# Performance work log

Hardware: AMD Instinct MI355X
Metric: run time of the kernel (lower is better)

The kernel has to match this reference:

```python
import jax, jax.numpy as jnp
import numpy as np

N = 100000
E = 1600000
IN_DIM = 64
EMB_DIM = 64
BN_EPS = 1e-5


def setup_inputs() -> dict:
    key = jax.random.key(0)
    ks = jax.random.split(key, 8)
    x = jax.random.normal(ks[0], (N, IN_DIM), dtype=jnp.float32)
    edge_index = jax.random.randint(ks[1], (2, E), 0, N, dtype=jnp.int64)
    # GIN learned epsilon (train_eps=True), initialized to 0 as in PyG
    eps = jnp.zeros((), dtype=jnp.float32)
    # MLP params: Linear(in, emb) -> BN -> ReLU -> Linear(emb, emb)
    s1 = 1.0 / np.sqrt(IN_DIM)
    W1 = jax.random.uniform(ks[2], (IN_DIM, EMB_DIM), jnp.float32, -s1, s1)
    b1 = jax.random.uniform(ks[3], (EMB_DIM,), jnp.float32, -s1, s1)
    gamma = jnp.ones((EMB_DIM,), jnp.float32)
    beta = jnp.zeros((EMB_DIM,), jnp.float32)
    s2 = 1.0 / np.sqrt(EMB_DIM)
    W2 = jax.random.uniform(ks[4], (EMB_DIM, EMB_DIM), jnp.float32, -s2, s2)
    b2 = jax.random.uniform(ks[5], (EMB_DIM,), jnp.float32, -s2, s2)
    return {"x": x, "edge_index": edge_index, "eps": eps,
            "W1": W1, "b1": b1, "gamma": gamma, "beta": beta,
            "W2": W2, "b2": b2}


def reference(x, edge_index, eps, W1, b1, gamma, beta, W2, b2):
    src, dst = edge_index[0], edge_index[1]
    # GIN aggregation: sum of neighbor (source) features at each destination
    agg = jax.ops.segment_sum(x[src], dst, num_segments=N)  # [N, IN_DIM]
    h = (1.0 + eps) * x + agg
    # MLP: Linear -> BatchNorm1d (training-mode batch stats) -> ReLU -> Linear
    h1 = h @ W1 + b1                                   # [N, EMB_DIM]
    mean = jnp.mean(h1, axis=0)
    var = jnp.mean((h1 - mean) ** 2, axis=0)           # biased var, as torch BN
    h1n = (h1 - mean) * jax.lax.rsqrt(var + BN_EPS) * gamma + beta
    h2 = jax.nn.relu(h1n)
    return h2 @ W2 + b2                                # [N, EMB_DIM]
```

## Files before the change

### kernel.cpp

```cpp
#include <hip/hip_runtime.h>

#define NNODES 100000
#define NEDGES 1600000
#define DIM 64
#define NB 782
#define NPB 256
#define CHUNK 6250
#define CAP 3968
#define HP 68
#define NTILES 6250

typedef __attribute__((ext_vector_type(4))) float f32x4;
typedef __attribute__((ext_vector_type(8))) short s16x8;

__device__ __forceinline__ unsigned short bf16_rne(float f) {
  unsigned u = __float_as_uint(f);
  u += 0x7FFF + ((u >> 16) & 1);
  return (unsigned short)(u >> 16);
}
__device__ __forceinline__ float bf16_to_f32(unsigned short h) {
  return __uint_as_float(((unsigned)h) << 16);
}

__global__ __launch_bounds__(256) void prep_kernel(
    const float* __restrict__ x, unsigned short* __restrict__ xb,
    int* __restrict__ gcursor, float* __restrict__ sums,
    const float* __restrict__ W1, const float* __restrict__ W2,
    unsigned short* __restrict__ Wp1, unsigned short* __restrict__ Wp2) {
  int i = blockIdx.x * 256 + threadIdx.x;
  float4 v = ((const float4*)x)[i];
  ushort4 o;
  o.x = bf16_rne(v.x); o.y = bf16_rne(v.y);
  o.z = bf16_rne(v.z); o.w = bf16_rne(v.w);
  ((ushort4*)xb)[i] = o;
  if (blockIdx.x == 0) {
    int t = threadIdx.x;
    for (int b = t; b < NB; b += 256) gcursor[b] = b * CAP;
    if (t < 2 * DIM) sums[t] = 0.0f;
    if (t < 128) {
      int lane = t & 63;
      const float* W = (t >= 64) ? W2 : W1;
      unsigned short* Wp = (t >= 64) ? Wp2 : Wp1;
      int q = lane >> 4, n16 = lane & 15;
#pragma unroll
      for (int f = 0; f < 8; ++f) {
        int kk = f >> 2, nt = f & 3;
#pragma unroll
        for (int j = 0; j < 8; ++j) {
          int k = kk * 32 + q * 8 + j;
          int n = nt * 16 + n16;
          Wp[f * 512 + lane * 8 + j] = bf16_rne(W[k * DIM + n]);
        }
      }
    }
  }
}

__global__ __launch_bounds__(1024) void partition_kernel(
    const int* __restrict__ ei, int* __restrict__ gcursor,
    int* __restrict__ bpart) {
  __shared__ int sd[1024];
  __shared__ int delta[1024];
  __shared__ int lcur[1024];
  __shared__ int stage[CHUNK];
  __shared__ unsigned short sbuck[CHUNK];
  int t = threadIdx.x;
  sd[t] = 0;
  __syncthreads();
  int base = blockIdx.x * CHUNK;
  for (int i = t; i < CHUNK; i += 1024)
    atomicAdd(&sd[ei[NEDGES + base + i] >> 7], 1);
  __syncthreads();
  int v = sd[t];
  for (int off = 1; off < 1024; off <<= 1) {
    int a = (t >= off) ? sd[t - off] : 0;
    __syncthreads();
    sd[t] += a;
    __syncthreads();
  }
  int excl = sd[t] - v;
  delta[t] = (v ? atomicAdd(&gcursor[t], v) : 0) - excl;
  lcur[t] = excl;
  __syncthreads();
  for (int i = t; i < CHUNK; i += 1024) {
    int s = ei[base + i];
    int d = ei[NEDGES + base + i];
    int b = d >> 7;
    int p = atomicAdd(&lcur[b], 1);
    stage[p] = ((d & 127) << 17) | s;
    sbuck[p] = (unsigned short)b;
  }
  __syncthreads();
  for (int i = t; i < CHUNK; i += 1024)
    bpart[delta[sbuck[i]] + i] = stage[i];
}

__global__ __launch_bounds__(512) void mega_kernel(
    const int* __restrict__ bpart, const int* __restrict__ gcursor,
    const unsigned short* __restrict__ xb, float* __restrict__ h1,
    const unsigned short* __restrict__ Wp, const float* __restrict__ b1,
    const float* __restrict__ epsp,
    float* __restrict__ sums, float* __restrict__ sumsq) {
  __shared__ int sd[128];
  __shared__ int cur[128];
  __shared__ int stage[CAP];
  __shared__ unsigned short hbuf[128 * HP];
  __shared__ float lsum[DIM];
  __shared__ float lsq[DIM];
  int b = blockIdx.x;
  int t = threadIdx.x;
  if (t < 128) sd[t] = 0;
  if (t < DIM) { lsum[t] = 0.0f; lsq[t] = 0.0f; }
  __syncthreads();
  int pbase = b * CAP;
  int cnt = gcursor[b] - pbase;
  for (int i = t; i < cnt; i += 512)
    atomicAdd(&sd[bpart[pbase + i] >> 17], 1);
  __syncthreads();
  int deg = (t < 128) ? sd[t] : 0;
  for (int off = 1; off < 128; off <<= 1) {
    int a = (t < 128 && t >= off) ? sd[t - off] : 0;
    __syncthreads();
    if (t < 128) sd[t] += a;
    __syncthreads();
  }
  if (t < 128) cur[t] = sd[t] - deg;
  __syncthreads();
  for (int i = t; i < cnt; i += 512) {
    int v = bpart[pbase + i];
    int p = atomicAdd(&cur[v >> 17], 1);
    stage[p] = v & 0x1FFFF;
  }
  __syncthreads();
  {
    int part = t & 15;
    int ng = t >> 4;
#pragma unroll 1
    for (int pass = 0; pass < 4; ++pass) {
      int nl = ng + pass * 32;
      int e0 = (nl == 0) ? 0 : sd[nl - 1];
      int e1 = sd[nl];
      float4 a0 = make_float4(0.f, 0.f, 0.f, 0.f);
      float4 a1 = a0, a2 = a0, a3 = a0;
      int e = e0;
      for (; e + 4 <= e1; e += 4) {
        int s0 = stage[e + 0];
        int s1 = stage[e + 1];
        int s2 = stage[e + 2];
        int s3 = stage[e + 3];
        ushort4 u0 = ((const ushort4*)(xb + (size_t)s0 * DIM))[part];
        ushort4 u1 = ((const ushort4*)(xb + (size_t)s1 * DIM))[part];
        ushort4 u2 = ((const ushort4*)(xb + (size_t)s2 * DIM))[part];
        ushort4 u3 = ((const ushort4*)(xb + (size_t)s3 * DIM))[part];
        a0.x += bf16_to_f32(u0.x); a0.y += bf16_to_f32(u0.y);
        a0.z += bf16_to_f32(u0.z); a0.w += bf16_to_f32(u0.w);
        a1.x += bf16_to_f32(u1.x); a1.y += bf16_to_f32(u1.y);
        a1.z += bf16_to_f32(u1.z); a1.w += bf16_to_f32(u1.w);
        a2.x += bf16_to_f32(u2.x); a2.y += bf16_to_f32(u2.y);
        a2.z += bf16_to_f32(u2.z); a2.w += bf16_to_f32(u2.w);
        a3.x += bf16_to_f32(u3.x); a3.y += bf16_to_f32(u3.y);
        a3.z += bf16_to_f32(u3.z); a3.w += bf16_to_f32(u3.w);
      }
      for (; e < e1; ++e) {
        int s = stage[e];
        ushort4 u = ((const ushort4*)(xb + (size_t)s * DIM))[part];
        a0.x += bf16_to_f32(u.x); a0.y += bf16_to_f32(u.y);
        a0.z += bf16_to_f32(u.z); a0.w += bf16_to_f32(u.w);
      }
      ushort4 o;
      o.x = bf16_rne((a0.x + a1.x) + (a2.x + a3.x));
      o.y = bf16_rne((a0.y + a1.y) + (a2.y + a3.y));
      o.z = bf16_rne((a0.z + a1.z) + (a2.z + a3.z));
      o.w = bf16_rne((a0.w + a1.w) + (a2.w + a3.w));
      *(ushort4*)&hbuf[nl * HP + part * 4] = o;
    }
  }
  __syncthreads();
  {
    int wave = t >> 6;
    int lane = t & 63;
    int tile = b * 8 + wave;
    if (tile < NTILES) {
      int q = lane >> 4;
      int r16 = lane & 15;
      float onep = 1.0f + epsp[0];
      s16x8 bf[8];
#pragma unroll
      for (int f = 0; f < 8; ++f)
        bf[f] = ((const s16x8*)Wp)[f * 64 + lane];
      int lrow = wave * 16 + r16;
      int grow = b * 128 + lrow;
      const s16x8* xrow = (const s16x8*)(xb + (size_t)grow * DIM);
      f32x4 acc[4] = {{0.f,0.f,0.f,0.f},{0.f,0.f,0.f,0.f},
                      {0.f,0.f,0.f,0.f},{0.f,0.f,0.f,0.f}};
#pragma unroll
      for (int kk = 0; kk < 2; ++kk) {
        s16x8 xv = xrow[kk * 4 + q];
        const unsigned short* hb = &hbuf[lrow * HP + kk * 32 + q * 8];
        ushort4 h0 = *(const ushort4*)hb;
        ushort4 h4 = *(const ushort4*)(hb + 4);
        s16x8 a;
        a[0] = (short)bf16_rne(fmaf(onep, bf16_to_f32((unsigned short)xv[0]), bf16_to_f32(h0.x)));
        a[1] = (short)bf16_rne(fmaf(onep, bf16_to_f32((unsigned short)xv[1]), bf16_to_f32(h0.y)));
        a[2] = (short)bf16_rne(fmaf(onep, bf16_to_f32((unsigned short)xv[2]), bf16_to_f32(h0.z)));
        a[3] = (short)bf16_rne(fmaf(onep, bf16_to_f32((unsigned short)xv[3]), bf16_to_f32(h0.w)));
        a[4] = (short)bf16_rne(fmaf(onep, bf16_to_f32((unsigned short)xv[4]), bf16_to_f32(h4.x)));
        a[5] = (short)bf16_rne(fmaf(onep, bf16_to_f32((unsigned short)xv[5]), bf16_to_f32(h4.y)));
        a[6] = (short)bf16_rne(fmaf(onep, bf16_to_f32((unsigned short)xv[6]), bf16_to_f32(h4.z)));
        a[7] = (short)bf16_rne(fmaf(onep, bf16_to_f32((unsigned short)xv[7]), bf16_to_f32(h4.w)));
#pragma unroll
        for (int nt = 0; nt < 4; ++nt)
          acc[nt] = __builtin_amdgcn_mfma_f32_16x16x32_bf16(
              a, bf[kk * 4 + nt], acc[nt], 0, 0, 0);
      }
      int orow = tile * 16 + q * 4;
#pragma unroll
      for (int nt = 0; nt < 4; ++nt) {
        int col = nt * 16 + r16;
        float bb = b1[col];
        float sl = 0.0f, ql = 0.0f;
#pragma unroll
        for (int r = 0; r < 4; ++r) {
          float v = acc[nt][r] + bb;
          h1[(size_t)(orow + r) * DIM + col] = v;
          sl += v;
          ql = fmaf(v, v, ql);
        }
        sl += __shfl_down(sl, 32); ql += __shfl_down(ql, 32);
        sl += __shfl_down(sl, 16); ql += __shfl_down(ql, 16);
        if (q == 0) {
          atomicAdd(&lsum[col], sl);
          atomicAdd(&lsq[col], ql);
        }
      }
    }
  }
  __syncthreads();
  if (t < DIM) {
    atomicAdd(&sums[t], lsum[t]);
    atomicAdd(&sumsq[t], lsq[t]);
  }
}

__global__ __launch_bounds__(256) void fused2_kernel(
    const float* __restrict__ h1, float* __restrict__ out,
    const unsigned short* __restrict__ Wp, const float* __restrict__ b2,
    const float* __restrict__ gamma, const float* __restrict__ beta,
    const float* __restrict__ sums, const float* __restrict__ sumsq) {
  __shared__ float sc_s[DIM];
  __shared__ float sh_s[DIM];
  int t = threadIdx.x;
  if (t < DIM) {
    float invN = 1.0f / (float)NNODES;
    float m = sums[t] * invN;
    float v = fmaf(-m, m, sumsq[t] * invN);
    float sc = gamma[t] * rsqrtf(v + 1e-5f);
    sc_s[t] = sc;
    sh_s[t] = fmaf(-m, sc, beta[t]);
  }
  __syncthreads();
  int wave = t >> 6;
  int lane = t & 63;
  int tile = blockIdx.x * 4 + wave;
  if (tile >= NTILES) return;
  int q = lane >> 4;
  int r16 = lane & 15;
  s16x8 bf[8];
#pragma unroll
  for (int f = 0; f < 8; ++f)
    bf[f] = ((const s16x8*)Wp)[f * 64 + lane];
  int arow = tile * 16 + r16;
  const float* hr = h1 + (size_t)arow * DIM + q * 8;
  f32x4 acc[4] = {{0.f,0.f,0.f,0.f},{0.f,0.f,0.f,0.f},
                  {0.f,0.f,0.f,0.f},{0.f,0.f,0.f,0.f}};
#pragma unroll
  for (int kk = 0; kk < 2; ++kk) {
    int kbase = kk * 32 + q * 8;
    float4 hv0 = *(const float4*)(hr + kk * 32);
    float4 hv1 = *(const float4*)(hr + kk * 32 + 4);
    float4 sc0 = *(const float4*)(sc_s + kbase);
    float4 sc1 = *(const float4*)(sc_s + kbase + 4);
    float4 sh0 = *(const float4*)(sh_s + kbase);
    float4 sh1 = *(const float4*)(sh_s + kbase + 4);
    s16x8 a;
    a[0] = (short)bf16_rne(fmaxf(fmaf(hv0.x, sc0.x, sh0.x), 0.f));
    a[1] = (short)bf16_rne(fmaxf(fmaf(hv0.y, sc0.y, sh0.y), 0.f));
    a[2] = (short)bf16_rne(fmaxf(fmaf(hv0.z, sc0.z, sh0.z), 0.f));
    a[3] = (short)bf16_rne(fmaxf(fmaf(hv0.w, sc0.w, sh0.w), 0.f));
    a[4] = (short)bf16_rne(fmaxf(fmaf(hv1.x, sc1.x, sh1.x), 0.f));
    a[5] = (short)bf16_rne(fmaxf(fmaf(hv1.y, sc1.y, sh1.y), 0.f));
    a[6] = (short)bf16_rne(fmaxf(fmaf(hv1.z, sc1.z, sh1.z), 0.f));
    a[7] = (short)bf16_rne(fmaxf(fmaf(hv1.w, sc1.w, sh1.w), 0.f));
#pragma unroll
    for (int nt = 0; nt < 4; ++nt)
      acc[nt] = __builtin_amdgcn_mfma_f32_16x16x32_bf16(
          a, bf[kk * 4 + nt], acc[nt], 0, 0, 0);
  }
  int orow = tile * 16 + q * 4;
#pragma unroll
  for (int nt = 0; nt < 4; ++nt) {
    int col = nt * 16 + r16;
    float bb = b2[col];
#pragma unroll
    for (int r = 0; r < 4; ++r)
      out[(size_t)(orow + r) * DIM + col] = acc[nt][r] + bb;
  }
}

extern "C" void kernel_launch(void* const* d_in, const int* in_sizes, int n_in,
                              void* d_out, int out_size, void* d_ws, size_t ws_size,
                              hipStream_t stream) {
  (void)in_sizes; (void)n_in; (void)out_size; (void)ws_size;
  const float* x     = (const float*)d_in[0];
  const int*   ei    = (const int*)d_in[1];
  const float* eps   = (const float*)d_in[2];
  const float* W1    = (const float*)d_in[3];
  const float* b1    = (const float*)d_in[4];
  const float* gamma = (const float*)d_in[5];
  const float* beta  = (const float*)d_in[6];
  const float* W2    = (const float*)d_in[7];
  const float* b2    = (const float*)d_in[8];
  float* outp = (float*)d_out;

  const int N = NNODES;

  float* h1      = (float*)d_ws;
  float* sums    = h1 + (size_t)N * DIM;
  float* sumsq   = sums + DIM;
  int*   gcursor = (int*)(sumsq + DIM);
  unsigned short* Wp1 = (unsigned short*)(gcursor + ((NB + 1) & ~1));
  unsigned short* Wp2 = Wp1 + 4096;
  int*            bpart = (int*)d_out;
  unsigned short* xb    = (unsigned short*)d_out + (size_t)NB * CAP * 2;

  prep_kernel     <<<N * DIM / 4 / 256, 256, 0, stream>>>(x, xb, gcursor, sums,
                                                          W1, W2, Wp1, Wp2);
  partition_kernel<<<NPB, 1024, 0, stream>>>(ei, gcursor, bpart);
  mega_kernel     <<<NB, 512, 0, stream>>>(bpart, gcursor, xb, h1,
                                           Wp1, b1, eps, sums, sumsq);
  fused2_kernel   <<<(NTILES + 3) / 4, 256, 0, stream>>>(h1, outp, Wp2, b2,
                                                         gamma, beta, sums, sumsq);
}
```

Baseline: 174.4 us.

## Merge prep and partition into one build kernel, memset cursors, unroll gather

```diff
diff --git a/kernel.cpp b/kernel.cpp
--- a/kernel.cpp
+++ b/kernel.cpp
@@ -6,6 +6,7 @@
 #define NB 782
 #define NPB 256
 #define CHUNK 6250
+#define NCONV 391
 #define CAP 3968
 #define HP 68
 #define NTILES 6250
@@ -22,21 +23,89 @@
   return __uint_as_float(((unsigned)h) << 16);
 }
 
-__global__ __launch_bounds__(256) void prep_kernel(
-    const float* __restrict__ x, unsigned short* __restrict__ xb,
-    int* __restrict__ gcursor, float* __restrict__ sums,
+__global__ __launch_bounds__(1024) void build_kernel(
+    const float* __restrict__ x, const int* __restrict__ ei,
+    int* __restrict__ gcursor, unsigned short* __restrict__ xb,
+    int* __restrict__ bpart,
     const float* __restrict__ W1, const float* __restrict__ W2,
     unsigned short* __restrict__ Wp1, unsigned short* __restrict__ Wp2) {
-  int i = blockIdx.x * 256 + threadIdx.x;
-  float4 v = ((const float4*)x)[i];
-  ushort4 o;
-  o.x = bf16_rne(v.x); o.y = bf16_rne(v.y);
-  o.z = bf16_rne(v.z); o.w = bf16_rne(v.w);
-  ((ushort4*)xb)[i] = o;
-  if (blockIdx.x == 0) {
-    int t = threadIdx.x;
-    for (int b = t; b < NB; b += 256) gcursor[b] = b * CAP;
-    if (t < 2 * DIM) sums[t] = 0.0f;
+  int t = threadIdx.x;
+  int bid = blockIdx.x;
+  if (bid < NPB) {
+    __shared__ int sd[1024];
+    __shared__ int delta[1024];
+    __shared__ int lcur[1024];
+    __shared__ int stage[CHUNK];
+    __shared__ unsigned short sbuck[CHUNK];
+    __shared__ int wsum[16];
+    sd[t] = 0;
+    __syncthreads();
+    int base = bid * CHUNK;
+    int vals[7], bks[7];
+#pragma unroll
+    for (int k = 0; k < 7; ++k) {
+      int i = t + k * 1024;
+      if (i < CHUNK) {
+        int s = ei[base + i];
+        int d = ei[NEDGES + base + i];
+        int b = d >> 7;
+        vals[k] = ((d & 127) << 17) | s;
+        bks[k] = b;
+        atomicAdd(&sd[b], 1);
+      }
+    }
+    __syncthreads();
+    int v = sd[t];
+    int lane = t & 63, wv = t >> 6;
+    int sv = v;
+#pragma unroll
+    for (int off = 1; off < 64; off <<= 1) {
+      int o = __shfl_up(sv, off);
+      if (lane >= off) sv += o;
+    }
+    if (lane == 63) wsum[wv] = sv;
+    __syncthreads();
+    if (wv == 0 && lane < 16) {
+      int w = wsum[lane];
+#pragma unroll
+      for (int off = 1; off < 16; off <<= 1) {
+        int o = __shfl_up(w, off);
+        if (lane >= off) w += o;
+      }
+      wsum[lane] = w;
+    }
+    __syncthreads();
+    int incl = sv + (wv ? wsum[wv - 1] : 0);
+    int excl = incl - v;
+    delta[t] = (v ? (t * CAP + atomicAdd(&gcursor[t], v)) : 0) - excl;
+    lcur[t] = excl;
+    __syncthreads();
+#pragma unroll
+    for (int k = 0; k < 7; ++k) {
+      int i = t + k * 1024;
+      if (i < CHUNK) {
+        int p = atomicAdd(&lcur[bks[k]], 1);
+        stage[p] = vals[k];
+        sbuck[p] = (unsigned short)bks[k];
+      }
+    }
+    __syncthreads();
+    for (int i = t; i < CHUNK; i += 1024)
+      bpart[delta[sbuck[i]] + i] = stage[i];
+  } else if (bid < NPB + NCONV) {
+    int cb = bid - NPB;
+#pragma unroll
+    for (int j = 0; j < 4; ++j) {
+      int i = cb * 4096 + j * 1024 + t;
+      if (i < NNODES * DIM / 4) {
+        float4 vv = ((const float4*)x)[i];
+        ushort4 o;
+        o.x = bf16_rne(vv.x); o.y = bf16_rne(vv.y);
+        o.z = bf16_rne(vv.z); o.w = bf16_rne(vv.w);
+        ((ushort4*)xb)[i] = o;
+      }
+    }
+  } else {
     if (t < 128) {
       int lane = t & 63;
       const float* W = (t >= 64) ? W2 : W1;
@@ -56,46 +125,7 @@
   }
 }
 
-__global__ __launch_bounds__(1024) void partition_kernel(
-    const int* __restrict__ ei, int* __restrict__ gcursor,
-    int* __restrict__ bpart) {
-  __shared__ int sd[1024];
-  __shared__ int delta[1024];
-  __shared__ int lcur[1024];
-  __shared__ int stage[CHUNK];
-  __shared__ unsigned short sbuck[CHUNK];
-  int t = threadIdx.x;
-  sd[t] = 0;
-  __syncthreads();
-  int base = blockIdx.x * CHUNK;
-  for (int i = t; i < CHUNK; i += 1024)
-    atomicAdd(&sd[ei[NEDGES + base + i] >> 7], 1);
-  __syncthreads();
-  int v = sd[t];
-  for (int off = 1; off < 1024; off <<= 1) {
-    int a = (t >= off) ? sd[t - off] : 0;
-    __syncthreads();
-    sd[t] += a;
-    __syncthreads();
-  }
-  int excl = sd[t] - v;
-  delta[t] = (v ? atomicAdd(&gcursor[t], v) : 0) - excl;
-  lcur[t] = excl;
-  __syncthreads();
-  for (int i = t; i < CHUNK; i += 1024) {
-    int s = ei[base + i];
-    int d = ei[NEDGES + base + i];
-    int b = d >> 7;
-    int p = atomicAdd(&lcur[b], 1);
-    stage[p] = ((d & 127) << 17) | s;
-    sbuck[p] = (unsigned short)b;
-  }
-  __syncthreads();
-  for (int i = t; i < CHUNK; i += 1024)
-    bpart[delta[sbuck[i]] + i] = stage[i];
-}
-
-__global__ __launch_bounds__(512) void mega_kernel(
+__global__ __launch_bounds__(512, 8) void mega_kernel(
     const int* __restrict__ bpart, const int* __restrict__ gcursor,
     const unsigned short* __restrict__ xb, float* __restrict__ h1,
     const unsigned short* __restrict__ Wp, const float* __restrict__ b1,
@@ -113,7 +143,7 @@
   if (t < DIM) { lsum[t] = 0.0f; lsq[t] = 0.0f; }
   __syncthreads();
   int pbase = b * CAP;
-  int cnt = gcursor[b] - pbase;
+  int cnt = gcursor[b];
   for (int i = t; i < cnt; i += 512)
     atomicAdd(&sd[bpart[pbase + i] >> 17], 1);
   __syncthreads();
@@ -143,6 +173,40 @@
       float4 a0 = make_float4(0.f, 0.f, 0.f, 0.f);
       float4 a1 = a0, a2 = a0, a3 = a0;
       int e = e0;
+      for (; e + 8 <= e1; e += 8) {
+        int s0 = stage[e + 0];
+        int s1 = stage[e + 1];
+        int s2 = stage[e + 2];
+        int s3 = stage[e + 3];
+        int s4 = stage[e + 4];
+        int s5 = stage[e + 5];
+        int s6 = stage[e + 6];
+        int s7 = stage[e + 7];
+        ushort4 u0 = ((const ushort4*)(xb + (size_t)s0 * DIM))[part];
+        ushort4 u1 = ((const ushort4*)(xb + (size_t)s1 * DIM))[part];
+        ushort4 u2 = ((const ushort4*)(xb + (size_t)s2 * DIM))[part];
+        ushort4 u3 = ((const ushort4*)(xb + (size_t)s3 * DIM))[part];
+        ushort4 u4 = ((const ushort4*)(xb + (size_t)s4 * DIM))[part];
+        ushort4 u5 = ((const ushort4*)(xb + (size_t)s5 * DIM))[part];
+        ushort4 u6 = ((const ushort4*)(xb + (size_t)s6 * DIM))[part];
+        ushort4 u7 = ((const ushort4*)(xb + (size_t)s7 * DIM))[part];
+        a0.x += bf16_to_f32(u0.x) + bf16_to_f32(u4.x);
+        a0.y += bf16_to_f32(u0.y) + bf16_to_f32(u4.y);
+        a0.z += bf16_to_f32(u0.z) + bf16_to_f32(u4.z);
+        a0.w += bf16_to_f32(u0.w) + bf16_to_f32(u4.w);
+        a1.x += bf16_to_f32(u1.x) + bf16_to_f32(u5.x);
+        a1.y += bf16_to_f32(u1.y) + bf16_to_f32(u5.y);
+        a1.z += bf16_to_f32(u1.z) + bf16_to_f32(u5.z);
+        a1.w += bf16_to_f32(u1.w) + bf16_to_f32(u5.w);
+        a2.x += bf16_to_f32(u2.x) + bf16_to_f32(u6.x);
+        a2.y += bf16_to_f32(u2.y) + bf16_to_f32(u6.y);
+        a2.z += bf16_to_f32(u2.z) + bf16_to_f32(u6.z);
+        a2.w += bf16_to_f32(u2.w) + bf16_to_f32(u6.w);
+        a3.x += bf16_to_f32(u3.x) + bf16_to_f32(u7.x);
+        a3.y += bf16_to_f32(u3.y) + bf16_to_f32(u7.y);
+        a3.z += bf16_to_f32(u3.z) + bf16_to_f32(u7.z);
+        a3.w += bf16_to_f32(u3.w) + bf16_to_f32(u7.w);
+      }
       for (; e + 4 <= e1; e += 4) {
         int s0 = stage[e + 0];
         int s1 = stage[e + 1];
@@ -328,16 +392,17 @@
   float* sums    = h1 + (size_t)N * DIM;
   float* sumsq   = sums + DIM;
   int*   gcursor = (int*)(sumsq + DIM);
-  unsigned short* Wp1 = (unsigned short*)(gcursor + ((NB + 1) & ~1));
+  unsigned short* Wp1 = (unsigned short*)(gcursor + 784);
   unsigned short* Wp2 = Wp1 + 4096;
   int*            bpart = (int*)d_out;
   unsigned short* xb    = (unsigned short*)d_out + (size_t)NB * CAP * 2;
 
-  prep_kernel     <<<N * DIM / 4 / 256, 256, 0, stream>>>(x, xb, gcursor, sums,
-                                                          W1, W2, Wp1, Wp2);
-  partition_kernel<<<NPB, 1024, 0, stream>>>(ei, gcursor, bpart);
-  mega_kernel     <<<NB, 512, 0, stream>>>(bpart, gcursor, xb, h1,
-                                           Wp1, b1, eps, sums, sumsq);
-  fused2_kernel   <<<(NTILES + 3) / 4, 256, 0, stream>>>(h1, outp, Wp2, b2,
-                                                         gamma, beta, sums, sumsq);
-}
+  hipMemsetAsync(sums, 0, (2 * DIM + NB) * sizeof(int), stream);
+
+  build_kernel<<<NPB + NCONV + 1, 1024, 0, stream>>>(x, ei, gcursor, xb, bpart,
+                                                     W1, W2, Wp1, Wp2);
+  mega_kernel <<<NB, 512, 0, stream>>>(bpart, gcursor, xb, h1,
+                                       Wp1, b1, eps, sums, sumsq);
+  fused2_kernel<<<(NTILES + 3) / 4, 256, 0, stream>>>(h1, outp, Wp2, b2,
+                                                      gamma, beta, sums, sumsq);
+}
```

New measurement: 175.9 us. About the same (+0.9%).
